# Kernel tuning notes

Measured on AMD Instinct MI355X. Metric: run time of the kernel, lower is better.

The kernel has to match this reference:

```python
import jax, jax.numpy as jnp
import numpy as np

EPS_NORM = 1e-12   # F.normalize eps
EPS_PERP = 1e-10   # perplexity log eps
COMMIT = 0.25


def _l2norm(x):
    # matches F.normalize(p=2, dim=1) with eps clamp
    n = jnp.sqrt(jnp.sum(x * x, axis=1, keepdims=True))
    return x / jnp.maximum(n, EPS_NORM)


def setup_inputs() -> dict:
    key = jax.random.key(0)
    k1, k2 = jax.random.split(key)
    B, D, L, K = 8, 256, 4096, 4096
    inputs = jax.random.normal(k1, (B, D, L), dtype=jnp.float32)
    # nn.Embedding init uniform(-1/K, 1/K); use uniform at that scale
    weight = jax.random.uniform(k2, (K, D), minval=-1.0 / K, maxval=1.0 / K, dtype=jnp.float32)
    return {"inputs": inputs, "weight": weight}


def reference(inputs, weight):
    K, D = weight.shape
    x = jnp.transpose(inputs, (0, 2, 1))          # [B, L, D]
    flat = x.reshape(-1, D)                       # [N, D]
    N = flat.shape[0]
    sim = _l2norm(flat) @ _l2norm(weight).T       # [N, K] cosine similarity
    # argmin(1 - sim) == argmax(sim)
    idx = jnp.argmax(sim, axis=1)                 # [N]
    # one-hot @ weight is just a gather of the selected code rows
    quantized = weight[idx].reshape(x.shape)      # [B, L, D]
    e_latent = jnp.mean((jax.lax.stop_gradient(quantized) - x) ** 2)
    q_latent = jnp.mean((quantized - jax.lax.stop_gradient(x)) ** 2)
    loss = q_latent + COMMIT * e_latent
    # straight-through estimator
    q_st = x + jax.lax.stop_gradient(quantized - x)
    # avg_probs = mean of one-hot encodings = normalized histogram of idx
    counts = jnp.zeros((K,), dtype=jnp.float32).at[idx].add(1.0)
    avg_probs = counts / N
    perplexity = jnp.exp(-jnp.sum(avg_probs * jnp.log(avg_probs + EPS_PERP)))
    return jnp.transpose(q_st, (0, 2, 1)), loss, perplexity
```

## Files before the change

kernel.cpp:

```cpp
#include <hip/hip_runtime.h>
#include <stdint.h>

#define Bb 8
#define Dd 256
#define Ll 4096
#define Kk 4096
#define Nn (Bb * Ll)
#define OUT0 (Bb * Dd * Ll)

typedef int    int4v   __attribute__((ext_vector_type(4)));
typedef int    int8v   __attribute__((ext_vector_type(8)));
typedef float  floatx4 __attribute__((ext_vector_type(4)));

#define SCALE1 0x7F7F7F7F

union V8 { int8v v; int4v h[2]; };

__device__ __forceinline__ void async_load16(const void* g, void* l) {
    __builtin_amdgcn_global_load_lds((const __attribute__((address_space(1))) void*)g,
                                     (__attribute__((address_space(3))) void*)l, 16, 0, 0);
}

__global__ void k_prep(const float* __restrict__ w, unsigned char* __restrict__ wn,
                       int* __restrict__ counts) {
    int blk = blockIdx.x, tid = threadIdx.x;
    if (blk == 0)
        for (int i = tid; i < Kk + 2; i += 256) counts[i] = 0;
    int row  = blk * 4 + (tid >> 6);
    int lane = tid & 63;
    float4 v = ((const float4*)(w + (size_t)row * Dd))[lane];
    float ss = v.x*v.x + v.y*v.y + v.z*v.z + v.w*v.w;
#pragma unroll
    for (int m = 1; m < 64; m <<= 1) ss += __shfl_xor(ss, m, 64);
    float s = 16.0f / fmaxf(sqrtf(ss), 1e-12f);
    int p = __builtin_amdgcn_cvt_pk_fp8_f32(v.x * s, v.y * s, 0, false);
    p     = __builtin_amdgcn_cvt_pk_fp8_f32(v.z * s, v.w * s, p, true);
    ((int*)(wn + (size_t)row * Dd))[lane] = p;
}

__global__ __launch_bounds__(256, 2) void k_gemm_argmax(
        const float* __restrict__ x, const unsigned char* __restrict__ Wn,
        unsigned int* __restrict__ keys) {
    __shared__ __align__(16) unsigned char As[128 * 256];
    __shared__ __align__(16) unsigned char Bs[2][64 * 256];
    __shared__ unsigned int red[128][2];

    int blk = blockIdx.x;
    int cg = blk & 1, bm = blk >> 1;
    int tid = threadIdx.x, lane = tid & 63, w = tid >> 6;
    int wm = w >> 1, wn = w & 1;
    int l15 = lane & 15, l4 = lane >> 4;

    int goff[4], loff[4];
#pragma unroll
    for (int j = 0; j < 4; ++j) {
        int q = j * 256 + tid;
        int col = q >> 4, p = q & 15;
        goff[j] = col * 256 + ((p ^ (col & 15)) << 4);
        loff[j] = q * 16;
    }
    const unsigned char* Wg = Wn + (size_t)cg * 2048 * 256;

#pragma unroll
    for (int j = 0; j < 4; ++j)
        async_load16(Wg + goff[j], (unsigned char*)Bs[0] + loff[j]);

    int b = bm >> 5, l0 = (bm & 31) * 128;
    const float* xs = x + (size_t)b * Dd * Ll + l0;
    int lg = tid & 31, dgr = tid >> 5;
#pragma unroll
    for (int i = 0; i < 8; ++i) {
        int d0 = dgr * 4 + i * 32;
        const float* s0 = xs + (size_t)d0 * Ll + lg * 4;
        float4 f0 = *(const float4*)(s0);
        float4 f1 = *(const float4*)(s0 + Ll);
        float4 f2 = *(const float4*)(s0 + 2 * (size_t)Ll);
        float4 f3 = *(const float4*)(s0 + 3 * (size_t)Ll);
#pragma unroll
        for (int jl = 0; jl < 4; ++jl) {
            float a0 = ((const float*)&f0)[jl], a1 = ((const float*)&f1)[jl];
            float a2 = ((const float*)&f2)[jl], a3 = ((const float*)&f3)[jl];
            int pk = __builtin_amdgcn_cvt_pk_fp8_f32(a0, a1, 0, false);
            pk     = __builtin_amdgcn_cvt_pk_fp8_f32(a2, a3, pk, true);
            int l = lg * 4 + jl;
            *(int*)(As + l * 256 + (((d0 >> 4) ^ (l & 15)) << 4) + (d0 & 15)) = pk;
        }
    }
    __syncthreads();

    int8v af[4][2];
#pragma unroll
    for (int fm = 0; fm < 4; ++fm)
#pragma unroll
        for (int ks = 0; ks < 2; ++ks) {
            int l = wm * 64 + fm * 16 + l15;
            int ch = ks * 8 + l4 * 2;
            V8 u;
            u.h[0] = *(const int4v*)(As + l * 256 + ((ch ^ l15) << 4));
            u.h[1] = *(const int4v*)(As + l * 256 + (((ch + 1) ^ l15) << 4));
            af[fm][ks] = u.v;
        }

    unsigned int rk[4][4];
#pragma unroll
    for (int fm = 0; fm < 4; ++fm)
#pragma unroll
        for (int r = 0; r < 4; ++r) rk[fm][r] = 0u;

    for (int cb = 0; cb < 32; ++cb) {
        int cur = cb & 1;
        if (cb < 31) {
            const unsigned char* g = Wg + (size_t)(cb + 1) * 64 * 256;
            unsigned char* lb = (unsigned char*)Bs[cur ^ 1];
#pragma unroll
            for (int j = 0; j < 4; ++j)
                async_load16(g + goff[j], lb + loff[j]);
        }
        const unsigned char* bb = (const unsigned char*)Bs[cur];
        int8v bf[2][2];
#pragma unroll
        for (int fn = 0; fn < 2; ++fn)
#pragma unroll
            for (int ks = 0; ks < 2; ++ks) {
                int col = wn * 32 + fn * 16 + l15;
                int ch = ks * 8 + l4 * 2;
                V8 u;
                u.h[0] = *(const int4v*)(bb + col * 256 + ((ch ^ l15) << 4));
                u.h[1] = *(const int4v*)(bb + col * 256 + (((ch + 1) ^ l15) << 4));
                bf[fn][ks] = u.v;
            }
        floatx4 acc[4][2];
#pragma unroll
        for (int fm = 0; fm < 4; ++fm)
#pragma unroll
            for (int fn = 0; fn < 2; ++fn) {
                floatx4 a = (floatx4)512.0f;
                a = __builtin_amdgcn_mfma_scale_f32_16x16x128_f8f6f4(
                        af[fm][0], bf[fn][0], a, 0, 0, 0, SCALE1, 0, SCALE1);
                a = __builtin_amdgcn_mfma_scale_f32_16x16x128_f8f6f4(
                        af[fm][1], bf[fn][1], a, 0, 0, 0, SCALE1, 0, SCALE1);
                acc[fm][fn] = a;
            }
        unsigned int i0 = (unsigned)(cb * 64 + wn * 32 + l15);
#pragma unroll
        for (int fm = 0; fm < 4; ++fm)
#pragma unroll
            for (int r = 0; r < 4; ++r) {
                unsigned int k0 = (__float_as_uint(acc[fm][0][r]) & 0xFFFFF000u) | i0;
                unsigned int k1 = (__float_as_uint(acc[fm][1][r]) & 0xFFFFF000u) | (i0 + 16u);
                unsigned int km = k0 > k1 ? k0 : k1;
                rk[fm][r] = rk[fm][r] > km ? rk[fm][r] : km;
            }
        __syncthreads();
    }

#pragma unroll
    for (int fm = 0; fm < 4; ++fm)
#pragma unroll
        for (int r = 0; r < 4; ++r) {
            unsigned int kx = rk[fm][r];
#pragma unroll
            for (int md = 1; md <= 8; md <<= 1) {
                unsigned int o = (unsigned int)__shfl_xor((int)kx, md, 64);
                kx = kx > o ? kx : o;
            }
            if (l15 == 0) red[wm * 64 + fm * 16 + l4 * 4 + r][wn] = kx;
        }
    __syncthreads();
    if (tid < 128) {
        unsigned int k0 = red[tid][0], k1 = red[tid][1];
        unsigned int kx = k0 > k1 ? k0 : k1;
        keys[(size_t)cg * Nn + bm * 128 + tid] = kx | ((unsigned)cg << 11);
    }
}

__global__ __launch_bounds__(256) void k_gather(
        const float* __restrict__ w, const float* __restrict__ x,
        const unsigned int* __restrict__ keys, float* __restrict__ out,
        int* __restrict__ counts) {
    __shared__ float wt[32][260];
    __shared__ int kidx[32];
    __shared__ float wsum[4];
    __shared__ int lastsh;
    float* lossacc = (float*)(counts + Kk);
    int*   done    = counts + Kk + 1;

    int blk = blockIdx.x, tid = threadIdx.x;
    int n0 = blk * 32;
    if (tid < 32) {
        unsigned int k0 = keys[n0 + tid], k1 = keys[Nn + n0 + tid];
        unsigned int kx = k0 > k1 ? k0 : k1;
        int ix = (int)(kx & 0xFFFu);
        kidx[tid] = ix;
        atomicAdd(&counts[ix], 1);
    }
    __syncthreads();
    int lane = tid & 63, wv = tid >> 6;
#pragma unroll
    for (int r8 = 0; r8 < 8; ++r8) {
        int r = wv * 8 + r8;
        float4 v = *(const float4*)(w + (size_t)kidx[r] * Dd + lane * 4);
        *(float4*)(&wt[r][lane * 4]) = v;
    }
    __syncthreads();

    int lq = tid & 7, dg = tid >> 3;
    int b = n0 >> 12, l0 = n0 & (Ll - 1);
    const float* xp = x   + (size_t)b * Dd * Ll + l0 + lq * 4;
    float*       op = out + (size_t)b * Dd * Ll + l0 + lq * 4;
    int r0 = lq * 4;
    float ls = 0.f;
#pragma unroll
    for (int i = 0; i < 8; ++i) {
        int d = i * 32 + dg;
        float4 xv = *(const float4*)(xp + (size_t)d * Ll);
        float4 qv = { wt[r0][d], wt[r0 + 1][d], wt[r0 + 2][d], wt[r0 + 3][d] };
        float d0 = qv.x - xv.x, d1 = qv.y - xv.y, d2 = qv.z - xv.z, d3 = qv.w - xv.w;
        ls += d0*d0 + d1*d1 + d2*d2 + d3*d3;
        *(float4*)(op + (size_t)d * Ll) = qv;
    }
#pragma unroll
    for (int m = 1; m < 64; m <<= 1) ls += __shfl_xor(ls, m, 64);
    if (lane == 0) wsum[wv] = ls;
    __syncthreads();
    if (tid == 0) {
        atomicAdd(lossacc, wsum[0] + wsum[1] + wsum[2] + wsum[3]);
        __threadfence();
        lastsh = (atomicAdd(done, 1) == 1023);
    }
    __syncthreads();
    if (lastsh) {
        __threadfence();
        float s = 0.f;
        for (int i = tid; i < Kk; i += 256) {
            float p = (float)counts[i] * (1.0f / Nn);
            s += p * logf(p + 1e-10f);
        }
#pragma unroll
        for (int m = 1; m < 64; m <<= 1) s += __shfl_xor(s, m, 64);
        if (lane == 0) wsum[wv] = s;
        __syncthreads();
        if (tid == 0) {
            out[OUT0]     = lossacc[0] * 1.25f / (float)OUT0;
            out[OUT0 + 1] = expf(-(wsum[0] + wsum[1] + wsum[2] + wsum[3]));
        }
    }
}

extern "C" void kernel_launch(void* const* d_in, const int* in_sizes, int n_in,
                              void* d_out, int out_size, void* d_ws, size_t ws_size,
                              hipStream_t stream) {
    const float* x = (const float*)d_in[0];
    const float* w = (const float*)d_in[1];
    float* out = (float*)d_out;
    char* ws = (char*)d_ws;

    unsigned char* wn   = (unsigned char*)ws;
    unsigned int*  keys = (unsigned int*)(ws + (1u << 20));
    int*           counts = (int*)(ws + (1u << 20) + (256u << 10));

    k_prep       <<<1024, 256, 0, stream>>>(w, wn, counts);
    k_gemm_argmax<<<512,  256, 0, stream>>>(x, wn, keys);
    k_gather     <<<1024, 256, 0, stream>>>(w, x, keys, out, counts);
}
```

Baseline: 180.3 us.

## Drop codebook split in GEMM-argmax and retile gather across row blocks

The GEMM-argmax kernel stops splitting the codebook into two halves across blocks. Each 512-thread block now scans all 4096 codes for its 128 rows with 128-column B tiles, so the x tile is loaded and converted to FP8 once instead of twice, and the two partial key arrays no longer have to be merged. The gather kernel now gives each block 128 rows by a quarter of D, using a padded stride-65 shared tile, and only one block per row group updates the histogram. The cost is one resident block per CU with larger LDS use (about 98 KB), fewer blocks to hide latency, and more waves in each reduction.

```diff
diff --git a/kernel.cpp b/kernel.cpp
--- a/kernel.cpp
+++ b/kernel.cpp
@@ -38,39 +38,37 @@
     ((int*)(wn + (size_t)row * Dd))[lane] = p;
 }
 
-__global__ __launch_bounds__(256, 2) void k_gemm_argmax(
+__global__ __launch_bounds__(512, 2) void k_gemm_argmax(
         const float* __restrict__ x, const unsigned char* __restrict__ Wn,
-        unsigned int* __restrict__ keys) {
+        int* __restrict__ idxout) {
     __shared__ __align__(16) unsigned char As[128 * 256];
-    __shared__ __align__(16) unsigned char Bs[2][64 * 256];
-    __shared__ unsigned int red[128][2];
-
-    int blk = blockIdx.x;
-    int cg = blk & 1, bm = blk >> 1;
+    __shared__ __align__(16) unsigned char Bs[2][128 * 256];
+    __shared__ unsigned int red[128][4];
+
+    int bm = blockIdx.x;
     int tid = threadIdx.x, lane = tid & 63, w = tid >> 6;
-    int wm = w >> 1, wn = w & 1;
+    int wm = w >> 2, wn = w & 3;
     int l15 = lane & 15, l4 = lane >> 4;
 
     int goff[4], loff[4];
 #pragma unroll
     for (int j = 0; j < 4; ++j) {
-        int q = j * 256 + tid;
+        int q = j * 512 + tid;
         int col = q >> 4, p = q & 15;
         goff[j] = col * 256 + ((p ^ (col & 15)) << 4);
         loff[j] = q * 16;
     }
-    const unsigned char* Wg = Wn + (size_t)cg * 2048 * 256;
 
 #pragma unroll
     for (int j = 0; j < 4; ++j)
-        async_load16(Wg + goff[j], (unsigned char*)Bs[0] + loff[j]);
+        async_load16(Wn + goff[j], (unsigned char*)Bs[0] + loff[j]);
 
     int b = bm >> 5, l0 = (bm & 31) * 128;
     const float* xs = x + (size_t)b * Dd * Ll + l0;
     int lg = tid & 31, dgr = tid >> 5;
 #pragma unroll
-    for (int i = 0; i < 8; ++i) {
-        int d0 = dgr * 4 + i * 32;
+    for (int i = 0; i < 4; ++i) {
+        int d0 = dgr * 4 + i * 64;
         const float* s0 = xs + (size_t)d0 * Ll + lg * 4;
         float4 f0 = *(const float4*)(s0);
         float4 f1 = *(const float4*)(s0 + Ll);
@@ -110,7 +108,7 @@
     for (int cb = 0; cb < 32; ++cb) {
         int cur = cb & 1;
         if (cb < 31) {
-            const unsigned char* g = Wg + (size_t)(cb + 1) * 64 * 256;
+            const unsigned char* g = Wn + (size_t)(cb + 1) * 128 * 256;
             unsigned char* lb = (unsigned char*)Bs[cur ^ 1];
 #pragma unroll
             for (int j = 0; j < 4; ++j)
@@ -141,7 +139,7 @@
                         af[fm][1], bf[fn][1], a, 0, 0, 0, SCALE1, 0, SCALE1);
                 acc[fm][fn] = a;
             }
-        unsigned int i0 = (unsigned)(cb * 64 + wn * 32 + l15);
+        unsigned int i0 = (unsigned)(cb * 128 + wn * 32 + l15);
 #pragma unroll
         for (int fm = 0; fm < 4; ++fm)
 #pragma unroll
@@ -169,52 +167,59 @@
     __syncthreads();
     if (tid < 128) {
         unsigned int k0 = red[tid][0], k1 = red[tid][1];
+        unsigned int k2 = red[tid][2], k3 = red[tid][3];
         unsigned int kx = k0 > k1 ? k0 : k1;
-        keys[(size_t)cg * Nn + bm * 128 + tid] = kx | ((unsigned)cg << 11);
+        kx = kx > k2 ? kx : k2;
+        kx = kx > k3 ? kx : k3;
+        idxout[bm * 128 + tid] = (int)(kx & 0xFFFu);
     }
 }
 
 __global__ __launch_bounds__(256) void k_gather(
         const float* __restrict__ w, const float* __restrict__ x,
-        const unsigned int* __restrict__ keys, float* __restrict__ out,
+        const int* __restrict__ idx, float* __restrict__ out,
         int* __restrict__ counts) {
-    __shared__ float wt[32][260];
-    __shared__ int kidx[32];
+    __shared__ float wt[128 * 65];
+    __shared__ int kidx[128];
     __shared__ float wsum[4];
     __shared__ int lastsh;
     float* lossacc = (float*)(counts + Kk);
     int*   done    = counts + Kk + 1;
 
     int blk = blockIdx.x, tid = threadIdx.x;
-    int n0 = blk * 32;
-    if (tid < 32) {
-        unsigned int k0 = keys[n0 + tid], k1 = keys[Nn + n0 + tid];
-        unsigned int kx = k0 > k1 ? k0 : k1;
-        int ix = (int)(kx & 0xFFFu);
+    int dq = blk & 3, lb = blk >> 2;
+    int n0 = lb * 128;
+    if (tid < 128) {
+        int ix = idx[n0 + tid];
         kidx[tid] = ix;
-        atomicAdd(&counts[ix], 1);
+        if (dq == 0) atomicAdd(&counts[ix], 1);
     }
     __syncthreads();
     int lane = tid & 63, wv = tid >> 6;
-#pragma unroll
-    for (int r8 = 0; r8 < 8; ++r8) {
-        int r = wv * 8 + r8;
-        float4 v = *(const float4*)(w + (size_t)kidx[r] * Dd + lane * 4);
-        *(float4*)(&wt[r][lane * 4]) = v;
-    }
-    __syncthreads();
-
-    int lq = tid & 7, dg = tid >> 3;
+    {
+        int rr = lane >> 4, c16 = lane & 15;
+#pragma unroll
+        for (int jr = 0; jr < 8; ++jr) {
+            int r = wv * 32 + jr * 4 + rr;
+            float4 v = *(const float4*)(w + (size_t)kidx[r] * Dd + dq * 64 + c16 * 4);
+            float* dst = &wt[r * 65 + c16 * 4];
+            dst[0] = v.x; dst[1] = v.y; dst[2] = v.z; dst[3] = v.w;
+        }
+    }
+    __syncthreads();
+
+    int lq = tid & 31, dg = tid >> 5;
     int b = n0 >> 12, l0 = n0 & (Ll - 1);
-    const float* xp = x   + (size_t)b * Dd * Ll + l0 + lq * 4;
-    float*       op = out + (size_t)b * Dd * Ll + l0 + lq * 4;
+    const float* xp = x   + ((size_t)b * Dd + dq * 64) * Ll + l0 + lq * 4;
+    float*       op = out + ((size_t)b * Dd + dq * 64) * Ll + l0 + lq * 4;
     int r0 = lq * 4;
     float ls = 0.f;
 #pragma unroll
     for (int i = 0; i < 8; ++i) {
-        int d = i * 32 + dg;
+        int d = i * 8 + dg;
         float4 xv = *(const float4*)(xp + (size_t)d * Ll);
-        float4 qv = { wt[r0][d], wt[r0 + 1][d], wt[r0 + 2][d], wt[r0 + 3][d] };
+        float4 qv = { wt[r0 * 65 + d],       wt[(r0 + 1) * 65 + d],
+                      wt[(r0 + 2) * 65 + d], wt[(r0 + 3) * 65 + d] };
         float d0 = qv.x - xv.x, d1 = qv.y - xv.y, d2 = qv.z - xv.z, d3 = qv.w - xv.w;
         ls += d0*d0 + d1*d1 + d2*d2 + d3*d3;
         *(float4*)(op + (size_t)d * Ll) = qv;
@@ -256,10 +261,10 @@
     char* ws = (char*)d_ws;
 
     unsigned char* wn   = (unsigned char*)ws;
-    unsigned int*  keys = (unsigned int*)(ws + (1u << 20));
-    int*           counts = (int*)(ws + (1u << 20) + (256u << 10));
+    int*           idx  = (int*)(ws + (1u << 20));
+    int*           counts = (int*)(ws + (1u << 20) + (128u << 10));
 
     k_prep       <<<1024, 256, 0, stream>>>(w, wn, counts);
-    k_gemm_argmax<<<512,  256, 0, stream>>>(x, wn, keys);
-    k_gather     <<<1024, 256, 0, stream>>>(w, x, keys, out, counts);
-}
+    k_gemm_argmax<<<256,  512, 0, stream>>>(x, wn, idx);
+    k_gather     <<<1024, 256, 0, stream>>>(w, x, idx, out, counts);
+}
```

Result: faster. 174.4 us (-3.3%).
